# Kernel tuning notes

Measured on AMD Instinct MI355X. Metric: run time of the kernel, lower is better.

Reference implementation:

```python
import jax, jax.numpy as jnp
import numpy as np

B, H, K, NUM_PTR, MAX_LEN = 32768, 896, 2000, 2, 128


def setup_inputs() -> dict:
    key = jax.random.key(0)
    k1, k2, k3 = jax.random.split(key, 3)
    z = jax.random.normal(k1, (B, H), dtype=jnp.float32)
    # codebook init: normal(0, 0.02) as in torch.nn.init.normal_
    emb = 0.02 * jax.random.normal(k2, (K, H), dtype=jnp.float32)
    # pointer heads: two Linear(H, MAX_LEN) layers, stacked
    W = jax.random.normal(k3, (NUM_PTR, MAX_LEN, H), dtype=jnp.float32) / np.float32(np.sqrt(H))
    b = jnp.zeros((NUM_PTR, MAX_LEN), dtype=jnp.float32)
    return {"z": z, "emb": emb, "W": W, "b": b, "prompt_len": 96}


def reference(z, emb, W, b, prompt_len):
    # --- quantize: L2 cdist + argmin + gather + straight-through ---
    # dist[b,k] = ||z_b||^2 - 2 z_b . e_k + ||e_k||^2   -> [B, K]
    dist = (jnp.sum(z * z, axis=1, keepdims=True)
            - 2.0 * (z @ emb.T)
            + jnp.sum(emb * emb, axis=1)[None, :])
    idx = jnp.argmin(dist, axis=1)            # [B]
    z_q = emb[idx]                            # [B, H]
    op_state = z + jax.lax.stop_gradient(z_q - z)
    # --- pointer heads with prompt-length mask ---
    logits = jnp.einsum('bh,plh->bpl', z, W) + b[None, :, :]   # [B, 2, MAX_LEN]
    mask = jnp.where(jnp.arange(logits.shape[-1]) < prompt_len, 0.0, -jnp.inf)
    ptr_logits = logits + mask[None, None, :]
    return op_state, ptr_logits
```

## Files before the change

kernel.cpp:

```cpp
#include <hip/hip_runtime.h>
#include <hip/hip_bf16.h>
#include <cstdint>
#include <cstddef>

#define B_SZ 32768
#define H_SZ 896
#define K_SZ 2000
#define KPAD 2048
#define NPTR_COLS 256
#define NCAT 2304
#define BM 256
#define BN 256
#define BK 32
#define NKS (H_SZ / BK)
#define NT_ARG 8

typedef float floatx4 __attribute__((ext_vector_type(4)));
typedef __bf16 bf16x8 __attribute__((ext_vector_type(8)));

#define MASK_NEG 1.0e30f

__device__ inline unsigned short f2bf_rne(float x) {
  unsigned u = __builtin_bit_cast(unsigned, x);
  unsigned r = u + 0x7fffu + ((u >> 16) & 1u);
  return (unsigned short)(r >> 16);
}
__device__ inline float bf2f(unsigned short b) {
  unsigned u = ((unsigned)b) << 16;
  return __builtin_bit_cast(float, u);
}

typedef __attribute__((address_space(1))) void GV;
typedef __attribute__((address_space(3))) void LV;
__device__ inline void load_lds16(const void* gsrc, void* ldst) {
  __builtin_amdgcn_global_load_lds((GV*)gsrc, (LV*)ldst, 16, 0, 0);
}

__global__ __launch_bounds__(256) void convert_all(
    const float* __restrict__ emb, const float* __restrict__ W,
    const float* __restrict__ z,
    unsigned short* __restrict__ cat_hi, unsigned short* __restrict__ cat_lo,
    float* __restrict__ normE,
    unsigned short* __restrict__ zhi, unsigned short* __restrict__ zlo) {
  const int bid = blockIdx.x;
  const int tid = threadIdx.x;
  if (bid < NCAT) {
    const int row = bid;
    const float* src = nullptr;
    bool zero = false;
    if (row < K_SZ)       src = emb + (size_t)row * H_SZ;
    else if (row < KPAD)  zero = true;
    else                  src = W + (size_t)(row - KPAD) * H_SZ;

    float ss = 0.f;
    for (int c = tid; c < H_SZ; c += 256) {
      float x = zero ? 0.f : src[c];
      unsigned short hb = f2bf_rne(x);
      float hf = bf2f(hb);
      unsigned short lb = f2bf_rne(x - hf);
      cat_hi[(size_t)row * H_SZ + c] = hb;
      cat_lo[(size_t)row * H_SZ + c] = lb;
      ss += x * x;
    }
    #pragma unroll
    for (int off = 32; off > 0; off >>= 1) ss += __shfl_down(ss, off);
    __shared__ float wsum[4];
    const int wave = tid >> 6, lane = tid & 63;
    if (lane == 0) wsum[wave] = ss;
    __syncthreads();
    if (tid == 0 && row < KPAD) normE[row] = wsum[0] + wsum[1] + wsum[2] + wsum[3];
  } else {
    const size_t t = (size_t)(bid - NCAT) * 256 + tid;
    const float* src = z + t * 8;
    float x[8];
    *(float4*)&x[0] = *(const float4*)src;
    *(float4*)&x[4] = *(const float4*)(src + 4);
    unsigned hv[4], lv[4];
    #pragma unroll
    for (int q = 0; q < 4; ++q) {
      unsigned short h0 = f2bf_rne(x[2 * q]), h1 = f2bf_rne(x[2 * q + 1]);
      float r0 = x[2 * q] - bf2f(h0), r1 = x[2 * q + 1] - bf2f(h1);
      unsigned short l0 = f2bf_rne(r0), l1 = f2bf_rne(r1);
      hv[q] = (unsigned)h0 | ((unsigned)h1 << 16);
      lv[q] = (unsigned)l0 | ((unsigned)l1 << 16);
    }
    *(uint4*)(zhi + t * 8) = make_uint4(hv[0], hv[1], hv[2], hv[3]);
    *(uint4*)(zlo + t * 8) = make_uint4(lv[0], lv[1], lv[2], lv[3]);
  }
}

__global__ __launch_bounds__(512, 2) void main_gemm(
    const unsigned short* __restrict__ zhi,
    const unsigned short* __restrict__ zlo,
    const unsigned short* __restrict__ cat_hi,
    const unsigned short* __restrict__ cat_lo,
    const float* __restrict__ normE,
    const float* __restrict__ bias,
    const int* __restrict__ plen_p,
    float* __restrict__ pmin, int* __restrict__ pidx,
    float* __restrict__ out_logits) {
  __shared__ unsigned short ldsA[2][2][BM * BK];
  __shared__ unsigned short ldsB[2][2][BN * BK];
  __shared__ float red_v[4][BM];
  __shared__ int   red_i[4][BM];

  const int tid = threadIdx.x;
  const int wave = tid >> 6, lane = tid & 63;
  const int wm = wave >> 2, wn = wave & 3;
  const int m0 = blockIdx.x * BM;
  const int nt = blockIdx.y;
  const int n0 = nt * BN;
  const int lrow = lane & 15, lk = lane >> 4;
  const int csw = ((lk ^ ((lrow >> 1) & 3)) << 3);

  const int srow = lane >> 2;
  const int scol = (((lane & 3) ^ ((lane >> 3) & 3)) << 3);

  size_t offA[2], offB[2];
  #pragma unroll
  for (int s = 0; s < 2; ++s) {
    const int seg = wave * 2 + s;
    offA[s] = (size_t)(m0 + seg * 16 + srow) * H_SZ + scol;
    offB[s] = (size_t)(n0 + seg * 16 + srow) * H_SZ + scol;
  }

  auto STAGE = [&](int b, int s, int kk) {
    const int seg = wave * 2 + s;
    load_lds16(zhi    + offA[s] + kk, &ldsA[b][0][seg * 512]);
    load_lds16(zlo    + offA[s] + kk, &ldsA[b][1][seg * 512]);
    load_lds16(cat_hi + offB[s] + kk, &ldsB[b][0][seg * 512]);
    load_lds16(cat_lo + offB[s] + kk, &ldsB[b][1][seg * 512]);
  };

  floatx4 acc[8][4];
  #pragma unroll
  for (int i = 0; i < 8; ++i)
    #pragma unroll
    for (int j = 0; j < 4; ++j) acc[i][j] = (floatx4){0.f, 0.f, 0.f, 0.f};

  bf16x8 ah[4], al[4], b0h[2], b0l[2], b1h[2], b1l[2];

  auto RD_A = [&](int b, int mhalf) {
    #pragma unroll
    for (int i = 0; i < 4; ++i) {
      const int r = (wm * 128 + (mhalf * 4 + i) * 16 + lrow) * BK + csw;
      ah[i] = *(const bf16x8*)&ldsA[b][0][r];
      al[i] = *(const bf16x8*)&ldsA[b][1][r];
    }
  };
  auto RD_B0 = [&](int b, int nhalf) {
    #pragma unroll
    for (int j = 0; j < 2; ++j) {
      const int r = (wn * 64 + (nhalf * 2 + j) * 16 + lrow) * BK + csw;
      b0h[j] = *(const bf16x8*)&ldsB[b][0][r];
      b0l[j] = *(const bf16x8*)&ldsB[b][1][r];
    }
  };
  auto RD_B1 = [&](int b, int nhalf) {
    #pragma unroll
    for (int j = 0; j < 2; ++j) {
      const int r = (wn * 64 + (nhalf * 2 + j) * 16 + lrow) * BK + csw;
      b1h[j] = *(const bf16x8*)&ldsB[b][0][r];
      b1l[j] = *(const bf16x8*)&ldsB[b][1][r];
    }
  };

  STAGE(0, 0, 0);
  STAGE(0, 1, 0);
  asm volatile("s_waitcnt vmcnt(0)" ::: "memory");
  __builtin_amdgcn_s_barrier();

  for (int ks = 0; ks < NKS; ++ks) {
    const int cur = ks & 1, nxt = cur ^ 1;
    const int kk1 = (ks + 1) * BK;
    const bool pf = (ks + 1 < NKS);

    RD_A(cur, 0);
    RD_B0(cur, 0);
    if (pf) STAGE(nxt, 0, kk1);
    __builtin_amdgcn_s_barrier();
    __builtin_amdgcn_s_setprio(1);
    #pragma unroll
    for (int i = 0; i < 4; ++i)
      #pragma unroll
      for (int j = 0; j < 2; ++j) {
        floatx4 c = acc[i][j];
        c = __builtin_amdgcn_mfma_f32_16x16x32_bf16(ah[i], b0h[j], c, 0, 0, 0);
        c = __builtin_amdgcn_mfma_f32_16x16x32_bf16(ah[i], b0l[j], c, 0, 0, 0);
        c = __builtin_amdgcn_mfma_f32_16x16x32_bf16(al[i], b0h[j], c, 0, 0, 0);
        acc[i][j] = c;
      }
    __builtin_amdgcn_s_setprio(0);
    __builtin_amdgcn_s_barrier();

    RD_B1(cur, 1);
    if (pf) STAGE(nxt, 1, kk1);
    __builtin_amdgcn_s_barrier();
    __builtin_amdgcn_s_setprio(1);
    #pragma unroll
    for (int i = 0; i < 4; ++i)
      #pragma unroll
      for (int j = 0; j < 2; ++j) {
        floatx4 c = acc[i][2 + j];
        c = __builtin_amdgcn_mfma_f32_16x16x32_bf16(ah[i], b1h[j], c, 0, 0, 0);
        c = __builtin_amdgcn_mfma_f32_16x16x32_bf16(ah[i], b1l[j], c, 0, 0, 0);
        c = __builtin_amdgcn_mfma_f32_16x16x32_bf16(al[i], b1h[j], c, 0, 0, 0);
        acc[i][2 + j] = c;
      }
    __builtin_amdgcn_s_setprio(0);
    __builtin_amdgcn_s_barrier();

    RD_A(cur, 1);
    __builtin_amdgcn_s_barrier();
    __builtin_amdgcn_s_setprio(1);
    #pragma unroll
    for (int i = 0; i < 4; ++i)
      #pragma unroll
      for (int j = 0; j < 2; ++j) {
        floatx4 c = acc[4 + i][2 + j];
        c = __builtin_amdgcn_mfma_f32_16x16x32_bf16(ah[i], b1h[j], c, 0, 0, 0);
        c = __builtin_amdgcn_mfma_f32_16x16x32_bf16(ah[i], b1l[j], c, 0, 0, 0);
        c = __builtin_amdgcn_mfma_f32_16x16x32_bf16(al[i], b1h[j], c, 0, 0, 0);
        acc[4 + i][2 + j] = c;
      }
    __builtin_amdgcn_s_setprio(0);
    __builtin_amdgcn_s_barrier();

    RD_B0(cur, 0);
    __builtin_amdgcn_s_barrier();
    __builtin_amdgcn_s_setprio(1);
    #pragma unroll
    for (int i = 0; i < 4; ++i)
      #pragma unroll
      for (int j = 0; j < 2; ++j) {
        floatx4 c = acc[4 + i][j];
        c = __builtin_amdgcn_mfma_f32_16x16x32_bf16(ah[i], b0h[j], c, 0, 0, 0);
        c = __builtin_amdgcn_mfma_f32_16x16x32_bf16(ah[i], b0l[j], c, 0, 0, 0);
        c = __builtin_amdgcn_mfma_f32_16x16x32_bf16(al[i], b0h[j], c, 0, 0, 0);
        acc[4 + i][j] = c;
      }
    __builtin_amdgcn_s_setprio(0);
    if (pf) { asm volatile("s_waitcnt vmcnt(0)" ::: "memory"); }
    __builtin_amdgcn_s_barrier();
    __builtin_amdgcn_sched_barrier(0);
  }

  if (nt < NT_ARG) {
    float nE[4]; bool valid[4]; int kcol[4];
    #pragma unroll
    for (int nj = 0; nj < 4; ++nj) {
      kcol[nj] = n0 + wn * 64 + nj * 16 + lrow;
      valid[nj] = (kcol[nj] < K_SZ);
      nE[nj] = normE[kcol[nj]];
    }
    #pragma unroll
    for (int mi = 0; mi < 8; ++mi) {
      #pragma unroll
      for (int r = 0; r < 4; ++r) {
        float v = 3.4e38f; int id = kcol[0];
        #pragma unroll
        for (int nj = 0; nj < 4; ++nj) {
          const float vv = valid[nj] ? (nE[nj] - 2.0f * acc[mi][nj][r]) : 3.4e38f;
          if (vv < v) { v = vv; id = kcol[nj]; }
        }
        #pragma unroll
        for (int m = 1; m < 16; m <<= 1) {
          const float ov = __shfl_xor(v, m);
          const int   oid = __shfl_xor(id, m);
          if (ov < v || (ov == v && oid < id)) { v = ov; id = oid; }
        }
        if (lrow == 0) {
          const int row_local = wm * 128 + mi * 16 + lk * 4 + r;
          red_v[wn][row_local] = v;
          red_i[wn][row_local] = id;
        }
      }
    }
    __syncthreads();
    if (tid < BM) {
      float v = red_v[0][tid]; int id = red_i[0][tid];
      #pragma unroll
      for (int w = 1; w < 4; ++w) {
        const float vw = red_v[w][tid];
        if (vw < v) { v = vw; id = red_i[w][tid]; }
      }
      pmin[(size_t)nt * B_SZ + m0 + tid] = v;
      pidx[(size_t)nt * B_SZ + m0 + tid] = id;
    }
  } else {
    const int plen = *plen_p;
    #pragma unroll
    for (int nj = 0; nj < 4; ++nj) {
      const int c = wn * 64 + nj * 16 + lrow;
      const float bv = bias[c];
      const bool masked = ((c & 127) >= plen);
      #pragma unroll
      for (int mi = 0; mi < 8; ++mi) {
        const int growbase = m0 + wm * 128 + mi * 16 + lk * 4;
        #pragma unroll
        for (int r = 0; r < 4; ++r) {
          const float val = masked ? -MASK_NEG : (acc[mi][nj][r] + bv);
          out_logits[(size_t)(growbase + r) * NPTR_COLS + c] = val;
        }
      }
    }
  }
}

__global__ __launch_bounds__(256) void merge_gather(
    const float* __restrict__ z, const float* __restrict__ emb,
    const float* __restrict__ pmin, const int* __restrict__ pidx,
    float* __restrict__ out0) {
  const int row = blockIdx.x;
  float v = pmin[row];
  int  id = pidx[row];
  #pragma unroll
  for (int t = 1; t < NT_ARG; ++t) {
    const float vt = pmin[(size_t)t * B_SZ + row];
    if (vt < v) { v = vt; id = pidx[(size_t)t * B_SZ + row]; }
  }
  const float4* e4 = (const float4*)(emb + (size_t)id * H_SZ);
  const float4* z4 = (const float4*)(z + (size_t)row * H_SZ);
  float4* o4 = (float4*)(out0 + (size_t)row * H_SZ);
  const int t = threadIdx.x;
  if (t < H_SZ / 4) {
    const float4 zz = z4[t], ee = e4[t];
    float4 r;
    r.x = zz.x + (ee.x - zz.x);
    r.y = zz.y + (ee.y - zz.y);
    r.z = zz.z + (ee.z - zz.z);
    r.w = zz.w + (ee.w - zz.w);
    o4[t] = r;
  }
}

extern "C" void kernel_launch(void* const* d_in, const int* in_sizes, int n_in,
                              void* d_out, int out_size, void* d_ws, size_t ws_size,
                              hipStream_t stream) {
  const float* z    = (const float*)d_in[0];
  const float* emb  = (const float*)d_in[1];
  const float* W    = (const float*)d_in[2];
  const float* bias = (const float*)d_in[3];
  const int*   plen = (const int*)d_in[4];
  float* out = (float*)d_out;

  char* ws = (char*)d_ws;
  unsigned short* cat_hi = (unsigned short*)(ws);
  unsigned short* cat_lo = (unsigned short*)(ws + 4128768);
  float* normE = (float*)(ws + 8257536);
  float* pmin  = (float*)(ws + 8265728);
  int*   pidx  = (int*)(ws + 9314304);

  unsigned short* zhi = (unsigned short*)out;
  unsigned short* zlo = zhi + (size_t)B_SZ * H_SZ;
  float* out_logits = out + (size_t)B_SZ * H_SZ;

  convert_all<<<dim3(NCAT + B_SZ * H_SZ / 2048), dim3(256), 0, stream>>>(
      emb, W, z, cat_hi, cat_lo, normE, zhi, zlo);
  main_gemm<<<dim3(B_SZ / BM, 9), dim3(512), 0, stream>>>(
      zhi, zlo, cat_hi, cat_lo, normE, bias, plen, pmin, pidx, out_logits);
  merge_gather<<<dim3(B_SZ), dim3(256), 0, stream>>>(z, emb, pmin, pidx, out);
}
```

Baseline: 668.5 us.

## Collapse ping-pong phase barriers into one barrier per K-step with register fragments

The main GEMM loop used to run four barrier-separated phases, reloading A and B fragments from LDS between them. It now reads the first A half and all four B fragments up front, issues both next-stage global-to-LDS copies together, and runs all MFMA blocks with only the second A half read mid-loop. A single barrier per K-step remains. This removes the intra-step barriers and redundant LDS re-reads of B0, at the cost of more live VGPRs (extra fragment registers) and a different interleaving of loads and MFMAs that the compiler must schedule.

```diff
diff --git a/kernel.cpp b/kernel.cpp
--- a/kernel.cpp
+++ b/kernel.cpp
@@ -138,33 +138,6 @@
     #pragma unroll
     for (int j = 0; j < 4; ++j) acc[i][j] = (floatx4){0.f, 0.f, 0.f, 0.f};
 
-  bf16x8 ah[4], al[4], b0h[2], b0l[2], b1h[2], b1l[2];
-
-  auto RD_A = [&](int b, int mhalf) {
-    #pragma unroll
-    for (int i = 0; i < 4; ++i) {
-      const int r = (wm * 128 + (mhalf * 4 + i) * 16 + lrow) * BK + csw;
-      ah[i] = *(const bf16x8*)&ldsA[b][0][r];
-      al[i] = *(const bf16x8*)&ldsA[b][1][r];
-    }
-  };
-  auto RD_B0 = [&](int b, int nhalf) {
-    #pragma unroll
-    for (int j = 0; j < 2; ++j) {
-      const int r = (wn * 64 + (nhalf * 2 + j) * 16 + lrow) * BK + csw;
-      b0h[j] = *(const bf16x8*)&ldsB[b][0][r];
-      b0l[j] = *(const bf16x8*)&ldsB[b][1][r];
-    }
-  };
-  auto RD_B1 = [&](int b, int nhalf) {
-    #pragma unroll
-    for (int j = 0; j < 2; ++j) {
-      const int r = (wn * 64 + (nhalf * 2 + j) * 16 + lrow) * BK + csw;
-      b1h[j] = *(const bf16x8*)&ldsB[b][0][r];
-      b1l[j] = *(const bf16x8*)&ldsB[b][1][r];
-    }
-  };
-
   STAGE(0, 0, 0);
   STAGE(0, 1, 0);
   asm volatile("s_waitcnt vmcnt(0)" ::: "memory");
@@ -175,71 +148,71 @@
     const int kk1 = (ks + 1) * BK;
     const bool pf = (ks + 1 < NKS);
 
-    RD_A(cur, 0);
-    RD_B0(cur, 0);
-    if (pf) STAGE(nxt, 0, kk1);
-    __builtin_amdgcn_s_barrier();
+    bf16x8 a1h[4], a1l[4], a2h[4], a2l[4], bh[4], bl[4];
+
+    #pragma unroll
+    for (int i = 0; i < 4; ++i) {
+      const int r = (wm * 128 + i * 16 + lrow) * BK + csw;
+      a1h[i] = *(const bf16x8*)&ldsA[cur][0][r];
+      a1l[i] = *(const bf16x8*)&ldsA[cur][1][r];
+    }
+    #pragma unroll
+    for (int j = 0; j < 4; ++j) {
+      const int r = (wn * 64 + j * 16 + lrow) * BK + csw;
+      bh[j] = *(const bf16x8*)&ldsB[cur][0][r];
+      bl[j] = *(const bf16x8*)&ldsB[cur][1][r];
+    }
+    if (pf) { STAGE(nxt, 0, kk1); STAGE(nxt, 1, kk1); }
+
     __builtin_amdgcn_s_setprio(1);
     #pragma unroll
     for (int i = 0; i < 4; ++i)
       #pragma unroll
       for (int j = 0; j < 2; ++j) {
         floatx4 c = acc[i][j];
-        c = __builtin_amdgcn_mfma_f32_16x16x32_bf16(ah[i], b0h[j], c, 0, 0, 0);
-        c = __builtin_amdgcn_mfma_f32_16x16x32_bf16(ah[i], b0l[j], c, 0, 0, 0);
-        c = __builtin_amdgcn_mfma_f32_16x16x32_bf16(al[i], b0h[j], c, 0, 0, 0);
+        c = __builtin_amdgcn_mfma_f32_16x16x32_bf16(a1h[i], bh[j], c, 0, 0, 0);
+        c = __builtin_amdgcn_mfma_f32_16x16x32_bf16(a1h[i], bl[j], c, 0, 0, 0);
+        c = __builtin_amdgcn_mfma_f32_16x16x32_bf16(a1l[i], bh[j], c, 0, 0, 0);
         acc[i][j] = c;
       }
-    __builtin_amdgcn_s_setprio(0);
-    __builtin_amdgcn_s_barrier();
-
-    RD_B1(cur, 1);
-    if (pf) STAGE(nxt, 1, kk1);
-    __builtin_amdgcn_s_barrier();
-    __builtin_amdgcn_s_setprio(1);
+    #pragma unroll
+    for (int i = 0; i < 4; ++i) {
+      const int r = (wm * 128 + (4 + i) * 16 + lrow) * BK + csw;
+      a2h[i] = *(const bf16x8*)&ldsA[cur][0][r];
+      a2l[i] = *(const bf16x8*)&ldsA[cur][1][r];
+    }
     #pragma unroll
     for (int i = 0; i < 4; ++i)
       #pragma unroll
       for (int j = 0; j < 2; ++j) {
         floatx4 c = acc[i][2 + j];
-        c = __builtin_amdgcn_mfma_f32_16x16x32_bf16(ah[i], b1h[j], c, 0, 0, 0);
-        c = __builtin_amdgcn_mfma_f32_16x16x32_bf16(ah[i], b1l[j], c, 0, 0, 0);
-        c = __builtin_amdgcn_mfma_f32_16x16x32_bf16(al[i], b1h[j], c, 0, 0, 0);
+        c = __builtin_amdgcn_mfma_f32_16x16x32_bf16(a1h[i], bh[2 + j], c, 0, 0, 0);
+        c = __builtin_amdgcn_mfma_f32_16x16x32_bf16(a1h[i], bl[2 + j], c, 0, 0, 0);
+        c = __builtin_amdgcn_mfma_f32_16x16x32_bf16(a1l[i], bh[2 + j], c, 0, 0, 0);
         acc[i][2 + j] = c;
       }
-    __builtin_amdgcn_s_setprio(0);
-    __builtin_amdgcn_s_barrier();
-
-    RD_A(cur, 1);
-    __builtin_amdgcn_s_barrier();
-    __builtin_amdgcn_s_setprio(1);
     #pragma unroll
     for (int i = 0; i < 4; ++i)
       #pragma unroll
       for (int j = 0; j < 2; ++j) {
         floatx4 c = acc[4 + i][2 + j];
-        c = __builtin_amdgcn_mfma_f32_16x16x32_bf16(ah[i], b1h[j], c, 0, 0, 0);
-        c = __builtin_amdgcn_mfma_f32_16x16x32_bf16(ah[i], b1l[j], c, 0, 0, 0);
-        c = __builtin_amdgcn_mfma_f32_16x16x32_bf16(al[i], b1h[j], c, 0, 0, 0);
+        c = __builtin_amdgcn_mfma_f32_16x16x32_bf16(a2h[i], bh[2 + j], c, 0, 0, 0);
+        c = __builtin_amdgcn_mfma_f32_16x16x32_bf16(a2h[i], bl[2 + j], c, 0, 0, 0);
+        c = __builtin_amdgcn_mfma_f32_16x16x32_bf16(a2l[i], bh[2 + j], c, 0, 0, 0);
         acc[4 + i][2 + j] = c;
       }
-    __builtin_amdgcn_s_setprio(0);
-    __builtin_amdgcn_s_barrier();
-
-    RD_B0(cur, 0);
-    __builtin_amdgcn_s_barrier();
-    __builtin_amdgcn_s_setprio(1);
     #pragma unroll
     for (int i = 0; i < 4; ++i)
       #pragma unroll
       for (int j = 0; j < 2; ++j) {
         floatx4 c = acc[4 + i][j];
-        c = __builtin_amdgcn_mfma_f32_16x16x32_bf16(ah[i], b0h[j], c, 0, 0, 0);
-        c = __builtin_amdgcn_mfma_f32_16x16x32_bf16(ah[i], b0l[j], c, 0, 0, 0);
-        c = __builtin_amdgcn_mfma_f32_16x16x32_bf16(al[i], b0h[j], c, 0, 0, 0);
+        c = __builtin_amdgcn_mfma_f32_16x16x32_bf16(a2h[i], bh[j], c, 0, 0, 0);
+        c = __builtin_amdgcn_mfma_f32_16x16x32_bf16(a2h[i], bl[j], c, 0, 0, 0);
+        c = __builtin_amdgcn_mfma_f32_16x16x32_bf16(a2l[i], bh[j], c, 0, 0, 0);
         acc[4 + i][j] = c;
       }
     __builtin_amdgcn_s_setprio(0);
+
     if (pf) { asm volatile("s_waitcnt vmcnt(0)" ::: "memory"); }
     __builtin_amdgcn_s_barrier();
     __builtin_amdgcn_sched_barrier(0);
```

New measurement: 669.9 us. About the same (+0.2%).
